# Kernel optimization log

Hardware: AMD Instinct MI355X
Metric: run time of the kernel (lower is better)

The kernel has to match this reference:

```python
import jax, jax.numpy as jnp
import numpy as np

B, T, DP, A = 1024, 256, 64, 8   # batch, num particles (seq len), particle dim, action dim
H = 256                          # recurr_size (GRU hidden)
HID = 256                        # MLP hidden
C = 2                            # num_critics
TIME_NORM = 100.0


def setup_inputs() -> dict:
    key = jax.random.key(0)
    ks = jax.random.split(key, 10)
    F = DP + 1        # features + weight channel
    DIN = H + A + 1   # encoding + action + time
    s = lambda k, shape: (jax.random.normal(k, shape, jnp.float32) * 0.05)
    return {
        "particles": jax.random.normal(ks[0], (B, T, DP), jnp.float32),
        "weights": jax.random.uniform(ks[1], (B, T), jnp.float32),
        "action": jax.random.normal(ks[2], (B, A), jnp.float32),
        "time_idx": jax.random.uniform(ks[3], (B,), jnp.float32) * TIME_NORM,
        # GRU params (flax GRUCell layout, gates fused as [r|z|n]):
        "Wi": s(ks[4], (F, 3 * H)),    # input kernel (ir|iz|in), with bias
        "bi": jnp.zeros((3 * H,), jnp.float32),
        "Wh": s(ks[5], (H, 3 * H)),    # hidden kernel (hr|hz|hn); only hn has bias
        "bhn": jnp.zeros((H,), jnp.float32),
        # Two MLPDecoder critics stacked on leading dim C:
        "W1": s(ks[6], (C, DIN, HID)),
        "b1": jnp.zeros((C, HID), jnp.float32),
        "W2": s(ks[7], (C, HID, HID)),
        "b2": jnp.zeros((C, HID), jnp.float32),
        "W3": s(ks[8], (C, HID, 1)),
        "b3": jnp.zeros((C, 1), jnp.float32),
    }


def reference(particles, weights, action, time_idx, Wi, bi, Wh, bhn, W1, b1, W2, b2, W3, b3):
    # feature_fn = identity; append particle weights as an extra channel
    inputs = jnp.concatenate([particles, weights[..., None]], axis=-1)  # [B,T,F]
    # Precompute all input projections (parallel over time), scan only the recurrence.
    xp = jnp.einsum('btf,fg->btg', inputs, Wi) + bi                     # [B,T,3H]
    xp = jnp.swapaxes(xp, 0, 1)                                         # [T,B,3H]
    h0 = jnp.zeros((inputs.shape[0], H), inputs.dtype)

    def step(h, x):
        hp = h @ Wh                                                     # [B,3H]
        r = jax.nn.sigmoid(x[:, :H] + hp[:, :H])
        z = jax.nn.sigmoid(x[:, H:2 * H] + hp[:, H:2 * H])
        n = jnp.tanh(x[:, 2 * H:] + r * (hp[:, 2 * H:] + bhn))
        h_new = (1.0 - z) * n + z * h
        return h_new, None

    h, _ = jax.lax.scan(step, h0, xp)                                   # last encoding [B,H]

    t = (time_idx / TIME_NORM)[:, None]                                 # [B,1]
    x = jnp.concatenate([h, action, t], axis=-1)                        # [B,DIN]

    # Both critic MLPs batched over leading critic dim C (ReLU hidden layers).
    h1 = jax.nn.relu(jnp.einsum('bd,cdh->cbh', x, W1) + b1[:, None, :])   # [C,B,HID]
    h2 = jax.nn.relu(jnp.einsum('cbh,chk->cbk', h1, W2) + b2[:, None, :]) # [C,B,HID]
    v = jnp.einsum('cbh,cho->cbo', h2, W3) + b3[:, None, :]               # [C,B,1]
    return jnp.moveaxis(v[..., 0], 0, -1)                               # [B,C]
```

## Files before the change

### kernel.cpp

```cpp
#include <hip/hip_runtime.h>


#define TSEQ 256
#define DPDIM 64

typedef float f32x4 __attribute__((ext_vector_type(4)));
typedef __bf16 bf16x8 __attribute__((ext_vector_type(8)));
typedef unsigned short ushort8 __attribute__((ext_vector_type(8)));

static __device__ __forceinline__ unsigned short f2bf(float f) {
  return __builtin_bit_cast(unsigned short, (__bf16)f);
}
static __device__ __forceinline__ float bf2f(unsigned short h) {
  return __builtin_bit_cast(float, ((unsigned)h) << 16);
}
static __device__ __forceinline__ float sigm(float x) {
  return __builtin_amdgcn_rcpf(1.f + __expf(-x));
}
static __device__ __forceinline__ float tanh_fast(float p) {
  float q = __expf(-2.f * fabsf(p));
  float t = (1.f - q) * __builtin_amdgcn_rcpf(1.f + q);
  return __builtin_bit_cast(float, __builtin_bit_cast(unsigned, t) |
                                   (__builtin_bit_cast(unsigned, p) & 0x80000000u));
}

#define OFF_WIT 0
#define OFF_XP  110592
#define OFF_H0  135168
#define OFF_H1  137888
#define OFF_BI  140608
#define OFF_W64 143680
#define LDS_GRU 146752

#define HSTRIDE 544

__global__ __launch_bounds__(512, 2) void gru_kernel(
    const float* __restrict__ particles, const float* __restrict__ weights,
    const float* __restrict__ Wi, const float* __restrict__ bi,
    const float* __restrict__ Wh, const float* __restrict__ bhn,
    unsigned short* __restrict__ hT)
{
  extern __shared__ char smem[];
  const int tid  = threadIdx.x;
  const int lane = tid & 63;
  const int w    = tid >> 6;
  const int l15  = lane & 15;
  const int kg   = lane >> 4;
  const int b0   = blockIdx.x * 4;

  for (int idx = tid; idx < 64 * 768; idx += 512) {
    int k = idx / 768, n = idx - k * 768;
    *(unsigned short*)(smem + OFF_WIT + n * 144 + k * 2) = f2bf(Wi[idx]);
  }
  for (int idx = tid; idx < 768; idx += 512) {
    *(float*)(smem + OFF_BI  + idx * 4) = bi[idx];
    *(float*)(smem + OFF_W64 + idx * 4) = Wi[64 * 768 + idx];
  }
  for (int idx = tid; idx < (2 * 5 * HSTRIDE) / 4; idx += 512)
    ((unsigned*)(smem + OFF_H0))[idx] = 0u;

  const int hcol0 = w * 16 + l15;
  const float bhn0 = bhn[hcol0];
  const float bhn1 = bhn[hcol0 + 128];

  bf16x8 whb[6][8];
  #pragma unroll
  for (int j = 0; j < 6; ++j) {
    const int tile = w + 8 * j;
    const float* wp = Wh + (size_t)(kg * 8) * 768 + tile * 16 + l15;
    #pragma unroll
    for (int ks = 0; ks < 8; ++ks) {
      ushort8 tmp;
      #pragma unroll
      for (int e = 0; e < 8; ++e)
        tmp[e] = f2bf(wp[(size_t)(ks * 32 + e) * 768]);
      whb[j][ks] = __builtin_bit_cast(bf16x8, tmp);
    }
  }
  __syncthreads();

  const unsigned arow = ((l15 & 3) == 0)
                      ? (unsigned)((l15 >> 2) * HSTRIDE + kg * 16)
                      : (unsigned)(4 * HSTRIDE + kg * 16);

  const float* pbase = particles +
      ((size_t)(b0 + (l15 >> 2)) * TSEQ + (l15 & 3)) * DPDIM + kg * 8;
  const float* wbase = weights + (size_t)(b0 + kg) * TSEQ;

  char* const xpb = smem + OFF_XP + hcol0 * 8 + kg * 2;

  f32x4 acc[6];
  const f32x4 fzero = {0.f, 0.f, 0.f, 0.f};
  float hreg0 = 0.f, hreg1 = 0.f;

  for (int g = 0; g < 64; ++g) {
    const int t0 = g * 4;

    #pragma unroll
    for (int j = 0; j < 6; ++j) acc[j] = fzero;
    #pragma unroll
    for (int ks = 0; ks < 2; ++ks) {
      const float* pp = pbase + (size_t)t0 * DPDIM + ks * 32;
      f32x4 pa = *(const f32x4*)pp;
      f32x4 pb = *(const f32x4*)(pp + 4);
      ushort8 tmp;
      tmp[0] = f2bf(pa[0]); tmp[1] = f2bf(pa[1]); tmp[2] = f2bf(pa[2]); tmp[3] = f2bf(pa[3]);
      tmp[4] = f2bf(pb[0]); tmp[5] = f2bf(pb[1]); tmp[6] = f2bf(pb[2]); tmp[7] = f2bf(pb[3]);
      bf16x8 af = __builtin_bit_cast(bf16x8, tmp);
      #pragma unroll
      for (int j = 0; j < 6; ++j) {
        const int n = hcol0 + 128 * j;
        bf16x8 bf = *(const bf16x8*)(smem + OFF_WIT + n * 144 + ks * 64 + kg * 16);
        acc[j] = __builtin_amdgcn_mfma_f32_16x16x32_bf16(af, bf, acc[j], 0, 0, 0);
      }
    }
    {
      f32x4 wv = *(const f32x4*)(wbase + t0);
      #pragma unroll
      for (int j = 0; j < 6; ++j) {
        const int col = hcol0 + 128 * j;
        const float biv  = *(const float*)(smem + OFF_BI  + col * 4);
        const float w64v = *(const float*)(smem + OFF_W64 + col * 4);
        #pragma unroll
        for (int r = 0; r < 4; ++r)
          *(unsigned short*)(xpb + j * 4096 + r * 1024) =
              f2bf(acc[j][r] + biv + wv[r] * w64v);
      }
    }

    #pragma unroll
    for (int tt = 0; tt < 4; ++tt) {
      const int t     = t0 + tt;
      const int rboff = (t & 1) ? OFF_H1 : OFF_H0;
      const int wboff = (t & 1) ? OFF_H0 : OFF_H1;
      #pragma unroll
      for (int j = 0; j < 6; ++j) acc[j] = fzero;
      const char* hb = smem + rboff;
      #pragma unroll
      for (int ks = 0; ks < 8; ++ks) {
        bf16x8 af = *(const bf16x8*)(hb + arow + ks * 64);
        #pragma unroll
        for (int j = 0; j < 6; ++j)
          acc[j] = __builtin_amdgcn_mfma_f32_16x16x32_bf16(af, whb[j][ks], acc[j], 0, 0, 0);
      }
      float xr0 = bf2f(*(const unsigned short*)(xpb + 0 * 4096 + tt * 1024));
      float xr1 = bf2f(*(const unsigned short*)(xpb + 1 * 4096 + tt * 1024));
      float xz0 = bf2f(*(const unsigned short*)(xpb + 2 * 4096 + tt * 1024));
      float xz1 = bf2f(*(const unsigned short*)(xpb + 3 * 4096 + tt * 1024));
      float xn0 = bf2f(*(const unsigned short*)(xpb + 4 * 4096 + tt * 1024));
      float xn1 = bf2f(*(const unsigned short*)(xpb + 5 * 4096 + tt * 1024));
      float rr0 = sigm(xr0 + acc[0][0]);
      float zz0 = sigm(xz0 + acc[2][0]);
      float nn0 = tanh_fast(xn0 + rr0 * (acc[4][0] + bhn0));
      unsigned short h0u = f2bf(nn0 + zz0 * (hreg0 - nn0));
      hreg0 = bf2f(h0u);
      float rr1 = sigm(xr1 + acc[1][0]);
      float zz1 = sigm(xz1 + acc[3][0]);
      float nn1 = tanh_fast(xn1 + rr1 * (acc[5][0] + bhn1));
      unsigned short h1u = f2bf(nn1 + zz1 * (hreg1 - nn1));
      hreg1 = bf2f(h1u);
      *(unsigned short*)(smem + wboff + kg * HSTRIDE + hcol0 * 2)         = h0u;
      *(unsigned short*)(smem + wboff + kg * HSTRIDE + (hcol0 + 128) * 2) = h1u;
      __syncthreads();
    }
  }

  hT[(size_t)(b0 + kg) * 256 + hcol0]       = f2bf(hreg0);
  hT[(size_t)(b0 + kg) * 256 + hcol0 + 128] = f2bf(hreg1);
}

#define HOFF_W1 0
#define HOFF_WT 135168
#define HOFF_H1 0
#define HOFF_W2 16896
#define HOFF_H2 135168
#define HOFF_B1 155648
#define HOFF_B2 156672
#define HOFF_W3 157696
#define LDS_HEAD 158720

#define HROWS 32

__global__ __launch_bounds__(512, 1) void head_kernel(
    const unsigned short* __restrict__ hT, const float* __restrict__ action,
    const float* __restrict__ time_idx, const float* __restrict__ W1,
    const float* __restrict__ b1, const float* __restrict__ W2,
    const float* __restrict__ b2, const float* __restrict__ W3,
    const float* __restrict__ b3, float* __restrict__ out)
{
  extern __shared__ char smem[];
  const int tid  = threadIdx.x;
  const int lane = tid & 63;
  const int w    = tid >> 6;
  const int l15  = lane & 15;
  const int kg   = lane >> 4;
  const int c    = blockIdx.x & 1;
  const int rt   = blockIdx.x >> 1;
  const int r0   = rt * HROWS;

  if (tid < 256) {
    *(float*)(smem + HOFF_B1 + tid * 4) = b1[c * 256 + tid];
    *(float*)(smem + HOFF_B2 + tid * 4) = b2[c * 256 + tid];
    *(float*)(smem + HOFF_W3 + tid * 4) = W3[c * 256 + tid];
  }
  for (int idx = tid; idx < 20480 / 4; idx += 512)
    ((unsigned*)(smem + HOFF_WT))[idx] = 0u;
  __syncthreads();

  for (int q = tid; q < 64 * 256; q += 512) {
    int k = q >> 6, n0 = (q & 63) * 4;
    f32x4 v = *(const f32x4*)(W1 + ((size_t)c * 265 + k) * 256 + n0);
    char* d = smem + HOFF_W1 + k * 2;
    *(unsigned short*)(d + (size_t)(n0 + 0) * 528) = f2bf(v[0]);
    *(unsigned short*)(d + (size_t)(n0 + 1) * 528) = f2bf(v[1]);
    *(unsigned short*)(d + (size_t)(n0 + 2) * 528) = f2bf(v[2]);
    *(unsigned short*)(d + (size_t)(n0 + 3) * 528) = f2bf(v[3]);
  }
  for (int idx = tid; idx < 9 * 256; idx += 512) {
    int kk = idx >> 8, n = idx & 255;
    *(unsigned short*)(smem + HOFF_WT + n * 80 + kk * 2) =
        f2bf(W1[((size_t)c * 265 + 256 + kk) * 256 + n]);
  }

  ushort8 atail[2];
  #pragma unroll
  for (int mt = 0; mt < 2; ++mt) {
    int row = r0 + mt * 16 + l15;
    ushort8 t8 = {0, 0, 0, 0, 0, 0, 0, 0};
    if (kg == 0) {
      f32x4 a0 = *(const f32x4*)(action + (size_t)row * 8);
      f32x4 a1 = *(const f32x4*)(action + (size_t)row * 8 + 4);
      t8[0] = f2bf(a0[0]); t8[1] = f2bf(a0[1]); t8[2] = f2bf(a0[2]); t8[3] = f2bf(a0[3]);
      t8[4] = f2bf(a1[0]); t8[5] = f2bf(a1[1]); t8[6] = f2bf(a1[2]); t8[7] = f2bf(a1[3]);
    } else if (kg == 1) {
      t8[0] = f2bf(time_idx[row] * 0.01f);
    }
    atail[mt] = t8;
  }
  __syncthreads();

  f32x4 acc[2][2];
  const f32x4 fzero = {0.f, 0.f, 0.f, 0.f};

  #pragma unroll
  for (int mt = 0; mt < 2; ++mt)
    #pragma unroll
    for (int i = 0; i < 2; ++i) acc[mt][i] = fzero;
  #pragma unroll
  for (int ks = 0; ks < 8; ++ks) {
    bf16x8 bfr0 = *(const bf16x8*)(smem + HOFF_W1 + ((w * 2 + 0) * 16 + l15) * 528 + ks * 64 + kg * 16);
    bf16x8 bfr1 = *(const bf16x8*)(smem + HOFF_W1 + ((w * 2 + 1) * 16 + l15) * 528 + ks * 64 + kg * 16);
    #pragma unroll
    for (int mt = 0; mt < 2; ++mt) {
      bf16x8 af = *(const bf16x8*)(hT + (size_t)(r0 + mt * 16 + l15) * 256 + ks * 32 + kg * 8);
      acc[mt][0] = __builtin_amdgcn_mfma_f32_16x16x32_bf16(af, bfr0, acc[mt][0], 0, 0, 0);
      acc[mt][1] = __builtin_amdgcn_mfma_f32_16x16x32_bf16(af, bfr1, acc[mt][1], 0, 0, 0);
    }
  }
  {
    bf16x8 bfr0 = *(const bf16x8*)(smem + HOFF_WT + ((w * 2 + 0) * 16 + l15) * 80 + kg * 16);
    bf16x8 bfr1 = *(const bf16x8*)(smem + HOFF_WT + ((w * 2 + 1) * 16 + l15) * 80 + kg * 16);
    #pragma unroll
    for (int mt = 0; mt < 2; ++mt) {
      bf16x8 af = __builtin_bit_cast(bf16x8, atail[mt]);
      acc[mt][0] = __builtin_amdgcn_mfma_f32_16x16x32_bf16(af, bfr0, acc[mt][0], 0, 0, 0);
      acc[mt][1] = __builtin_amdgcn_mfma_f32_16x16x32_bf16(af, bfr1, acc[mt][1], 0, 0, 0);
    }
  }
  __syncthreads();

  #pragma unroll
  for (int mt = 0; mt < 2; ++mt)
    #pragma unroll
    for (int i = 0; i < 2; ++i) {
      int col = (w * 2 + i) * 16 + l15;
      float bv = *(const float*)(smem + HOFF_B1 + col * 4);
      #pragma unroll
      for (int r = 0; r < 4; ++r) {
        float v = acc[mt][i][r] + bv; v = v > 0.f ? v : 0.f;
        *(unsigned short*)(smem + HOFF_H1 + (mt * 16 + kg * 4 + r) * 528 + col * 2) = f2bf(v);
      }
    }
  for (int q = tid; q < 64 * 256; q += 512) {
    int k = q >> 6, n0 = (q & 63) * 4;
    f32x4 v = *(const f32x4*)(W2 + ((size_t)c * 256 + k) * 256 + n0);
    char* d = smem + HOFF_W2 + k * 2;
    *(unsigned short*)(d + (size_t)(n0 + 0) * 528) = f2bf(v[0]);
    *(unsigned short*)(d + (size_t)(n0 + 1) * 528) = f2bf(v[1]);
    *(unsigned short*)(d + (size_t)(n0 + 2) * 528) = f2bf(v[2]);
    *(unsigned short*)(d + (size_t)(n0 + 3) * 528) = f2bf(v[3]);
  }
  __syncthreads();

  #pragma unroll
  for (int mt = 0; mt < 2; ++mt)
    #pragma unroll
    for (int i = 0; i < 2; ++i) acc[mt][i] = fzero;
  #pragma unroll
  for (int ks = 0; ks < 8; ++ks) {
    bf16x8 bfr0 = *(const bf16x8*)(smem + HOFF_W2 + ((w * 2 + 0) * 16 + l15) * 528 + ks * 64 + kg * 16);
    bf16x8 bfr1 = *(const bf16x8*)(smem + HOFF_W2 + ((w * 2 + 1) * 16 + l15) * 528 + ks * 64 + kg * 16);
    #pragma unroll
    for (int mt = 0; mt < 2; ++mt) {
      bf16x8 af = *(const bf16x8*)(smem + HOFF_H1 + (mt * 16 + l15) * 528 + ks * 64 + kg * 16);
      acc[mt][0] = __builtin_amdgcn_mfma_f32_16x16x32_bf16(af, bfr0, acc[mt][0], 0, 0, 0);
      acc[mt][1] = __builtin_amdgcn_mfma_f32_16x16x32_bf16(af, bfr1, acc[mt][1], 0, 0, 0);
    }
  }
  __syncthreads();

  #pragma unroll
  for (int mt = 0; mt < 2; ++mt)
    #pragma unroll
    for (int i = 0; i < 2; ++i) {
      int col = (w * 2 + i) * 16 + l15;
      float bv = *(const float*)(smem + HOFF_B2 + col * 4);
      #pragma unroll
      for (int r = 0; r < 4; ++r) {
        float v = acc[mt][i][r] + bv; v = v > 0.f ? v : 0.f;
        *(unsigned short*)(smem + HOFF_H2 + (mt * 16 + kg * 4 + r) * 528 + col * 2) = f2bf(v);
      }
    }
  __syncthreads();

  {
    int row = tid >> 2, q = tid & 3;
    if (row < HROWS) {
      float s = 0.f;
      #pragma unroll
      for (int i = 0; i < 16; ++i) {
        uint2 hh = *(const uint2*)(smem + HOFF_H2 + row * 528 + (q * 64 + i * 4) * 2);
        const float* w3p = (const float*)(smem + HOFF_W3) + q * 64 + i * 4;
        s += bf2f((unsigned short)hh.x)         * w3p[0];
        s += bf2f((unsigned short)(hh.x >> 16)) * w3p[1];
        s += bf2f((unsigned short)hh.y)         * w3p[2];
        s += bf2f((unsigned short)(hh.y >> 16)) * w3p[3];
      }
      s += __shfl_xor(s, 1);
      s += __shfl_xor(s, 2);
      if (q == 0) out[(r0 + row) * 2 + c] = s + b3[c];
    }
  }
}

extern "C" void kernel_launch(void* const* d_in, const int* in_sizes, int n_in,
                              void* d_out, int out_size, void* d_ws, size_t ws_size,
                              hipStream_t stream) {
  const float* particles = (const float*)d_in[0];
  const float* weights   = (const float*)d_in[1];
  const float* action    = (const float*)d_in[2];
  const float* time_idx  = (const float*)d_in[3];
  const float* Wi        = (const float*)d_in[4];
  const float* bi        = (const float*)d_in[5];
  const float* Wh        = (const float*)d_in[6];
  const float* bhn       = (const float*)d_in[7];
  const float* W1        = (const float*)d_in[8];
  const float* b1        = (const float*)d_in[9];
  const float* W2        = (const float*)d_in[10];
  const float* b2        = (const float*)d_in[11];
  const float* W3        = (const float*)d_in[12];
  const float* b3        = (const float*)d_in[13];
  unsigned short* hT = (unsigned short*)d_ws;
  float* out = (float*)d_out;

  (void)hipFuncSetAttribute((const void*)gru_kernel,
                            hipFuncAttributeMaxDynamicSharedMemorySize, LDS_GRU);
  (void)hipFuncSetAttribute((const void*)head_kernel,
                            hipFuncAttributeMaxDynamicSharedMemorySize, LDS_HEAD);

  hipLaunchKernelGGL(gru_kernel, dim3(256), dim3(512), LDS_GRU, stream,
                     particles, weights, Wi, bi, Wh, bhn, hT);
  hipLaunchKernelGGL(head_kernel, dim3(64), dim3(512), LDS_HEAD, stream,
                     hT, action, time_idx, W1, b1, W2, b2, W3, b3, out);
}
```

Before: 649.4 us.

## Prefetch particle chunks into LDS asynchronously with double buffering

Each 4-step group's particle tile is now loaded by wave 0 with global_load_lds into a double-buffered, XOR-swizzled LDS region one group ahead, instead of every wave issuing direct global loads inside the recurrence loop. The particle weights for the block are also staged once into LDS up front. The aim is to take global-memory latency off the serial GRU critical path. In exchange it uses more LDS, which may reduce occupancy, and correctness depends on the existing barriers in the time loop ordering the async LDS writes before they are read.

```diff
diff --git a/kernel.cpp b/kernel.cpp
--- a/kernel.cpp
+++ b/kernel.cpp
@@ -22,6 +22,11 @@
   float t = (1.f - q) * __builtin_amdgcn_rcpf(1.f + q);
   return __builtin_bit_cast(float, __builtin_bit_cast(unsigned, t) |
                                    (__builtin_bit_cast(unsigned, p) & 0x80000000u));
+}
+static __device__ __forceinline__ void gload_lds16(const float* g, char* l) {
+  __builtin_amdgcn_global_load_lds(
+      (const __attribute__((address_space(1))) unsigned int*)g,
+      (__attribute__((address_space(3))) unsigned int*)l, 16, 0, 0);
 }
 
 #define OFF_WIT 0
@@ -30,7 +35,9 @@
 #define OFF_H1  137888
 #define OFF_BI  140608
 #define OFF_W64 143680
-#define LDS_GRU 146752
+#define OFF_P   146752
+#define OFF_W   154944
+#define LDS_GRU 159040
 
 #define HSTRIDE 544
 
@@ -48,6 +55,16 @@
   const int kg   = lane >> 4;
   const int b0   = blockIdx.x * 4;
 
+  if (w == 0) {
+    #pragma unroll
+    for (int i = 0; i < 4; ++i) {
+      int r = i * 4 + (lane >> 4);
+      int s = (lane & 15) ^ (r & 7);
+      const float* src = particles +
+          ((size_t)(b0 + (r >> 2)) * TSEQ + (r & 3)) * DPDIM + s * 4;
+      gload_lds16(src, smem + OFF_P + i * 1024);
+    }
+  }
   for (int idx = tid; idx < 64 * 768; idx += 512) {
     int k = idx / 768, n = idx - k * 768;
     *(unsigned short*)(smem + OFF_WIT + n * 144 + k * 2) = f2bf(Wi[idx]);
@@ -56,6 +73,9 @@
     *(float*)(smem + OFF_BI  + idx * 4) = bi[idx];
     *(float*)(smem + OFF_W64 + idx * 4) = Wi[64 * 768 + idx];
   }
+  for (int idx = tid; idx < 1024; idx += 512)
+    *(float*)(smem + OFF_W + idx * 4) =
+        weights[(size_t)(b0 + (idx >> 8)) * TSEQ + (idx & 255)];
   for (int idx = tid; idx < (2 * 5 * HSTRIDE) / 4; idx += 512)
     ((unsigned*)(smem + OFF_H0))[idx] = 0u;
 
@@ -83,10 +103,6 @@
                       ? (unsigned)((l15 >> 2) * HSTRIDE + kg * 16)
                       : (unsigned)(4 * HSTRIDE + kg * 16);
 
-  const float* pbase = particles +
-      ((size_t)(b0 + (l15 >> 2)) * TSEQ + (l15 & 3)) * DPDIM + kg * 8;
-  const float* wbase = weights + (size_t)(b0 + kg) * TSEQ;
-
   char* const xpb = smem + OFF_XP + hcol0 * 8 + kg * 2;
 
   f32x4 acc[6];
@@ -96,13 +112,26 @@
   for (int g = 0; g < 64; ++g) {
     const int t0 = g * 4;
 
+    if (w == 0 && g < 63) {
+      char* dst = smem + OFF_P + (((g + 1) & 1) << 12);
+      #pragma unroll
+      for (int i = 0; i < 4; ++i) {
+        int r = i * 4 + (lane >> 4);
+        int s = (lane & 15) ^ (r & 7);
+        const float* src = particles +
+            ((size_t)(b0 + (r >> 2)) * TSEQ + (t0 + 4 + (r & 3))) * DPDIM + s * 4;
+        gload_lds16(src, dst + i * 1024);
+      }
+    }
+
+    const char* pl = smem + OFF_P + ((g & 1) << 12) + l15 * 256;
     #pragma unroll
     for (int j = 0; j < 6; ++j) acc[j] = fzero;
     #pragma unroll
     for (int ks = 0; ks < 2; ++ks) {
-      const float* pp = pbase + (size_t)t0 * DPDIM + ks * 32;
-      f32x4 pa = *(const f32x4*)pp;
-      f32x4 pb = *(const f32x4*)(pp + 4);
+      const int bs = ks * 8 + kg * 2;
+      f32x4 pa = *(const f32x4*)(pl + (((bs + 0) ^ (l15 & 7)) * 16));
+      f32x4 pb = *(const f32x4*)(pl + (((bs + 1) ^ (l15 & 7)) * 16));
       ushort8 tmp;
       tmp[0] = f2bf(pa[0]); tmp[1] = f2bf(pa[1]); tmp[2] = f2bf(pa[2]); tmp[3] = f2bf(pa[3]);
       tmp[4] = f2bf(pb[0]); tmp[5] = f2bf(pb[1]); tmp[6] = f2bf(pb[2]); tmp[7] = f2bf(pb[3]);
@@ -115,7 +144,7 @@
       }
     }
     {
-      f32x4 wv = *(const f32x4*)(wbase + t0);
+      f32x4 wv = *(const f32x4*)(smem + OFF_W + kg * 1024 + t0 * 4);
       #pragma unroll
       for (int j = 0; j < 6; ++j) {
         const int col = hcol0 + 128 * j;
```

Result: slower. 1.439 ms (+121.6%).
